# Performance work log

Hardware: AMD Instinct MI355X
Metric: run time of the kernel (lower is better)

The kernel has to match this reference:

```python
import jax, jax.numpy as jnp
import numpy as np

N, E, G = 20000, 320000, 64
IN_DIM, HID, HEADS, NCLS = 512, 256, 2, 10
EPS = 1e-5
SLOPE = 0.2


def setup_inputs() -> dict:
    key = jax.random.key(0)
    ks = jax.random.split(key, 24)
    s = 0.02
    inp = {
        "feat": jax.random.normal(ks[0], (N, IN_DIM), jnp.float32),
        "src": jax.random.randint(ks[1], (E,), 0, N, jnp.int32),
        "dst": jax.random.randint(ks[2], (E,), 0, N, jnp.int32),
        "graph_ids": jnp.sort(jax.random.randint(ks[3], (N,), 0, G, jnp.int32)),
        # GATv2Conv params (fc_src, fc_dst, attn)
        "W_src": jax.random.normal(ks[4], (IN_DIM, HEADS * HID), jnp.float32) * s,
        "b_src": jnp.zeros((HEADS * HID,), jnp.float32),
        "W_dst": jax.random.normal(ks[5], (IN_DIM, HEADS * HID), jnp.float32) * s,
        "b_dst": jnp.zeros((HEADS * HID,), jnp.float32),
        "attn": jax.random.normal(ks[6], (HEADS, HID), jnp.float32) * s,
        # skip_lin: input_dim -> 2*hidden
        "W_skip": jax.random.normal(ks[7], (IN_DIM, 2 * HID), jnp.float32) * s,
        "b_skip": jnp.zeros((2 * HID,), jnp.float32),
        # bn1 affine
        "gamma": jnp.ones((2 * HID,), jnp.float32),
        "beta": jnp.zeros((2 * HID,), jnp.float32),
        # dim_reducer
        "W_red": jax.random.normal(ks[8], (2 * HID, HID), jnp.float32) * s,
        "b_red": jnp.zeros((HID,), jnp.float32),
        # attention-pool gate Linear(hidden, 1)
        "w_gate": jax.random.normal(ks[9], (HID, 1), jnp.float32) * s,
        "b_gate": jnp.zeros((1,), jnp.float32),
        # classifier MLP
        "W1": jax.random.normal(ks[10], (HID, HID // 2), jnp.float32) * s,
        "b1": jnp.zeros((HID // 2,), jnp.float32),
        "W2": jax.random.normal(ks[11], (HID // 2, NCLS), jnp.float32) * s,
        "b2": jnp.zeros((NCLS,), jnp.float32),
    }
    return inp


def _gatv2(feat, src, dst, W_src, b_src, W_dst, b_dst, attn):
    # feat_src/feat_dst: [N, H, D]
    fs = (feat @ W_src + b_src).reshape(N, HEADS, HID)
    fd = (feat @ W_dst + b_dst).reshape(N, HEADS, HID)
    fs_e = fs[src]                               # [E, H, D]
    m = jax.nn.leaky_relu(fs_e + fd[dst], SLOPE)  # [E, H, D]
    e = jnp.einsum("ehd,hd->eh", m, attn)         # [E, H]
    # edge softmax grouped by destination node
    e_max = jax.ops.segment_max(e, dst, num_segments=N)          # [N, H]
    e_exp = jnp.exp(e - e_max[dst])                               # [E, H]
    denom = jax.ops.segment_sum(e_exp, dst, num_segments=N)      # [N, H]
    alpha = e_exp / denom[dst]                                    # [E, H]
    out = jax.ops.segment_sum(alpha[:, :, None] * fs_e, dst, num_segments=N)
    return out  # [N, H, D]; zero rows for zero in-degree nodes


def reference(feat, src, dst, graph_ids, W_src, b_src, W_dst, b_dst, attn,
              W_skip, b_skip, gamma, beta, W_red, b_red, w_gate, b_gate,
              W1, b1, W2, b2):
    h1 = jax.nn.elu(_gatv2(feat, src, dst, W_src, b_src, W_dst, b_dst, attn))
    h1 = h1.reshape(N, HEADS * HID)
    h1 = h1 + (feat @ W_skip + b_skip)
    # BatchNorm1d (training-mode batch statistics, biased variance)
    mu = jnp.mean(h1, axis=0)
    var = jnp.mean((h1 - mu) ** 2, axis=0)
    h1 = (h1 - mu) * jax.lax.rsqrt(var + EPS) * gamma + beta
    hr = h1 @ W_red + b_red                      # [N, HID]
    # GlobalAttentionPooling: segment softmax of gate scores over each graph
    gate = hr @ w_gate + b_gate                  # [N, 1]
    g_max = jax.ops.segment_max(gate, graph_ids, num_segments=G)
    g_exp = jnp.exp(gate - g_max[graph_ids])
    g_den = jax.ops.segment_sum(g_exp, graph_ids, num_segments=G)
    a = g_exp / g_den[graph_ids]                 # [N, 1]
    h_g = jax.ops.segment_sum(a * hr, graph_ids, num_segments=G)  # [G, HID]
    # classifier (dropout = identity at inference)
    return jax.nn.relu(h_g @ W1 + b1) @ W2 + b2  # [G, NCLS]
```

## Files before the change

### kernel.cpp

```cpp
#include <hip/hip_runtime.h>
#include <math.h>

#define N_NODES 20000
#define N_EDGES 320000
#define N_GRAPH 64
#define IN_DIM  512
#define HID     256
#define F2      512
#define EPS_BN  1e-5f
#define SLOPE   0.2f
#define SCAN_BLOCKS 79
#define N_RT    157
#define RT_PAD  20096

typedef unsigned short u16;
typedef __attribute__((ext_vector_type(8))) short bf16x8;
typedef __attribute__((ext_vector_type(4))) float floatx4;

__device__ __forceinline__ u16 bf_hi(float x) {
    unsigned int u = __float_as_uint(x);
    return (u16)((u + 0x7fffu + ((u >> 16) & 1u)) >> 16);
}
__device__ __forceinline__ float bf_val(u16 h) {
    return __uint_as_float((unsigned int)h << 16);
}
__device__ __forceinline__ void unpack2(unsigned int u, float& lo, float& hi) {
    lo = __uint_as_float(u << 16);
    hi = __uint_as_float(u & 0xffff0000u);
}
__device__ __forceinline__ float lr(float x) { return fmaxf(x, SLOPE * x); }

__global__ void init_zero_kernel(int* counts, int* cursor, float* stats,
                                 float* h_gnum, float* gden, float* gate) {
    int i = blockIdx.x * blockDim.x + threadIdx.x;
    if (i < N_NODES) { counts[i] = 0; cursor[i] = 0; gate[i] = 0.f; }
    if (i < 1024) stats[i] = 0.f;
    if (i < N_GRAPH * HID) h_gnum[i] = 0.f;
    if (i < N_GRAPH) gden[i] = 0.f;
}

__global__ __launch_bounds__(256) void split_feat_kernel(
    const float* __restrict__ X, u16* __restrict__ Hi, int total8, int pad8) {
    int i = blockIdx.x * 256 + threadIdx.x;
    if (i >= pad8) return;
    size_t base = (size_t)i * 8;
    if (i >= total8) {
        *(uint4*)(Hi + base) = make_uint4(0, 0, 0, 0);
        return;
    }
    float4 x0 = *(const float4*)(X + base);
    float4 x1 = *(const float4*)(X + base + 4);
    float xs[8] = {x0.x, x0.y, x0.z, x0.w, x1.x, x1.y, x1.z, x1.w};
    union { u16 s[8]; uint4 v; } h;
#pragma unroll
    for (int j = 0; j < 8; j++) h.s[j] = bf_hi(xs[j]);
    *(uint4*)(Hi + base) = h.v;
}

__global__ __launch_bounds__(256) void split_wt_kernel(
    const float* __restrict__ Ws, const float* __restrict__ Wd,
    const float* __restrict__ Wk, const float* __restrict__ Wr,
    u16* __restrict__ Hi, u16* __restrict__ Lo) {
    __shared__ float t[32][33];
    int w = blockIdx.z;
    int ncols = (w == 3) ? 256 : 512;
    int n0 = blockIdx.y * 32;
    if (n0 >= ncols) return;
    const float* W = (w == 0) ? Ws : ((w == 1) ? Wd : ((w == 2) ? Wk : Wr));
    size_t obase = (size_t)w * 512 * 512;
    int k0 = blockIdx.x * 32;
    int tx = threadIdx.x, ty = threadIdx.y;
#pragma unroll
    for (int i = 0; i < 4; i++)
        t[ty * 4 + i][tx] = W[(size_t)(k0 + ty * 4 + i) * ncols + n0 + tx];
    __syncthreads();
#pragma unroll
    for (int i = 0; i < 4; i++) {
        float x = t[tx][ty * 4 + i];
        u16 hh = bf_hi(x);
        size_t o = obase + (size_t)(n0 + ty * 4 + i) * 512 + k0 + tx;
        Hi[o] = hh;
        Lo[o] = bf_hi(x - bf_val(hh));
    }
}

__global__ __launch_bounds__(256) void gemm_mfma_triple(
    const u16* __restrict__ Fhi, const u16* __restrict__ Wthi,
    const float* __restrict__ b_src, const float* __restrict__ b_dst,
    const float* __restrict__ b_skip,
    u16* __restrict__ FS16, u16* __restrict__ FD16,
    u16* __restrict__ h1hi, u16* __restrict__ h1lo) {
    __shared__ u16 As[2][128 * 72];
    int b = blockIdx.x;
    int xcd = b & 7, slot = b >> 3;
    int rt = (slot / 12) * 8 + xcd;
    if (rt >= N_RT) return;
    int cw = slot % 12;
    int w_idx = cw >> 2;
    int col0 = (cw & 3) * 128;
    int row0 = rt * 128;
    int tid = threadIdx.x;
    int lane = tid & 63, wave = tid >> 6;
    int wm = (wave & 1) * 64, wn = (wave >> 1) * 64;
    int quad = lane >> 4, l16 = lane & 15;

    int sr = tid >> 1, sh = (tid & 1) * 32;
    const u16* gA = Fhi + (size_t)(row0 + sr) * 512 + sh;
    int sOff = sr * 72 + sh;

    const u16* Wb = Wthi + (size_t)w_idx * 512 * 512;
    const u16* bP[4];
#pragma unroll
    for (int nt = 0; nt < 4; nt++)
        bP[nt] = Wb + (size_t)(col0 + wn + nt * 16 + l16) * 512 + quad * 8;

    floatx4 acc[4][4];
#pragma unroll
    for (int i = 0; i < 4; i++)
#pragma unroll
        for (int j = 0; j < 4; j++) acc[i][j] = (floatx4){0.f, 0.f, 0.f, 0.f};

    union { uint4 u; bf16x8 v; } bcur[8], bnxt[8];
    {
        uint4 a0 = *(const uint4*)(gA + 0);
        uint4 a1 = *(const uint4*)(gA + 8);
        uint4 a2 = *(const uint4*)(gA + 16);
        uint4 a3 = *(const uint4*)(gA + 24);
#pragma unroll
        for (int nt = 0; nt < 4; nt++) {
            bcur[nt * 2 + 0].u = *(const uint4*)(bP[nt] + 0);
            bcur[nt * 2 + 1].u = *(const uint4*)(bP[nt] + 32);
        }
        *(uint4*)(&As[0][sOff + 0])  = a0;
        *(uint4*)(&As[0][sOff + 8])  = a1;
        *(uint4*)(&As[0][sOff + 16]) = a2;
        *(uint4*)(&As[0][sOff + 24]) = a3;
    }
    __syncthreads();

    for (int kk = 0; kk < 8; kk++) {
        uint4 na0, na1, na2, na3;
        bool more = kk < 7;
        if (more) {
            int k1 = (kk + 1) * 64;
            na0 = *(const uint4*)(gA + k1 + 0);
            na1 = *(const uint4*)(gA + k1 + 8);
            na2 = *(const uint4*)(gA + k1 + 16);
            na3 = *(const uint4*)(gA + k1 + 24);
#pragma unroll
            for (int nt = 0; nt < 4; nt++) {
                bnxt[nt * 2 + 0].u = *(const uint4*)(bP[nt] + k1 + 0);
                bnxt[nt * 2 + 1].u = *(const uint4*)(bP[nt] + k1 + 32);
            }
        }
        const u16* base = &As[kk & 1][0];
#pragma unroll
        for (int s = 0; s < 2; s++) {
#pragma unroll
            for (int mt = 0; mt < 4; mt++) {
                bf16x8 ah = *(const bf16x8*)&base[(wm + mt * 16 + l16) * 72 + s * 32 + quad * 8];
#pragma unroll
                for (int nt = 0; nt < 4; nt++)
                    acc[mt][nt] = __builtin_amdgcn_mfma_f32_16x16x32_bf16(ah, bcur[nt * 2 + s].v, acc[mt][nt], 0, 0, 0);
            }
        }
        if (more) {
            u16* d = &As[(kk + 1) & 1][sOff];
            *(uint4*)(d + 0)  = na0;
            *(uint4*)(d + 8)  = na1;
            *(uint4*)(d + 16) = na2;
            *(uint4*)(d + 24) = na3;
            __syncthreads();
#pragma unroll
            for (int i = 0; i < 8; i++) bcur[i] = bnxt[i];
        }
    }

    const float* bias = (w_idx == 0) ? b_src : ((w_idx == 1) ? b_dst : b_skip);
    float bv[4];
#pragma unroll
    for (int nt = 0; nt < 4; nt++) bv[nt] = bias[col0 + wn + nt * 16 + l16];
#pragma unroll
    for (int mt = 0; mt < 4; mt++) {
#pragma unroll
        for (int r = 0; r < 4; r++) {
            int m = row0 + wm + mt * 16 + quad * 4 + r;
            if (m < N_NODES) {
#pragma unroll
                for (int nt = 0; nt < 4; nt++) {
                    int n = col0 + wn + nt * 16 + l16;
                    float vv = acc[mt][nt][r] + bv[nt];
                    if (w_idx == 0)      FS16[(size_t)m * 512 + n] = bf_hi(vv);
                    else if (w_idx == 1) FD16[(size_t)m * 512 + n] = bf_hi(vv);
                    else {
                        u16 hh = bf_hi(vv);
                        h1hi[(size_t)m * 512 + n] = hh;
                        h1lo[(size_t)m * 512 + n] = bf_hi(vv - bf_val(hh));
                    }
                }
            }
        }
    }
}

__global__ void hist_kernel(const int* __restrict__ dst, int* __restrict__ counts) {
    int e = blockIdx.x * blockDim.x + threadIdx.x;
    if (e < N_EDGES) atomicAdd(&counts[dst[e]], 1);
}

__global__ __launch_bounds__(256) void scan_local_kernel(
    const int* __restrict__ counts, int* __restrict__ row_ptr, int* __restrict__ bsum) {
    __shared__ int buf[256];
    int b = blockIdx.x, tid = threadIdx.x;
    int i = b * 256 + tid;
    buf[tid] = (i < N_NODES) ? counts[i] : 0;
    __syncthreads();
    for (int off = 1; off < 256; off <<= 1) {
        int t = (tid >= off) ? buf[tid - off] : 0;
        __syncthreads();
        buf[tid] += t;
        __syncthreads();
    }
    if (i < N_NODES) row_ptr[i + 1] = buf[tid];
    if (tid == 255) bsum[b] = buf[255];
}

__global__ __launch_bounds__(256) void scan_fixup_kernel(
    const int* __restrict__ bsum, int* __restrict__ row_ptr) {
    __shared__ int red[256];
    int b = blockIdx.x, tid = threadIdx.x;
    red[tid] = (tid < b) ? bsum[tid] : 0;
    __syncthreads();
    for (int off = 128; off > 0; off >>= 1) {
        if (tid < off) red[tid] += red[tid + off];
        __syncthreads();
    }
    int offset = red[0];
    int i = b * 256 + tid;
    if (i < N_NODES) row_ptr[i + 1] += offset;
    if (b == 0 && tid == 0) row_ptr[0] = 0;
}

__global__ void scatter_kernel(const int* __restrict__ src, const int* __restrict__ dst,
                               const int* __restrict__ row_ptr,
                               int* __restrict__ cursor, int* __restrict__ csr_src) {
    int e = blockIdx.x * blockDim.x + threadIdx.x;
    if (e < N_EDGES) {
        int d = dst[e];
        int pos = atomicAdd(&cursor[d], 1);
        csr_src[row_ptr[d] + pos] = src[e];
    }
}

__global__ __launch_bounds__(256) void edge_fused_kernel(
    const u16* __restrict__ FS16, const u16* __restrict__ FD16,
    const float* __restrict__ attn, const int* __restrict__ csr_src,
    const int* __restrict__ row_ptr,
    u16* __restrict__ h1hi, u16* __restrict__ h1lo) {
    __shared__ float red[3 * 512];
    __shared__ float den[2];
    int n = blockIdx.x, tid = threadIdx.x;
    int lane = tid & 63, wave = tid >> 6;
    int beg = row_ptr[n], end = row_ptr[n + 1], deg = end - beg;
    if (tid < 2) den[tid] = 0.f;

    float fdv[8], aw[8];
    {
        uint4 q = *(const uint4*)(FD16 + (size_t)n * 512 + 8 * lane);
        unpack2(q.x, fdv[0], fdv[1]); unpack2(q.y, fdv[2], fdv[3]);
        unpack2(q.z, fdv[4], fdv[5]); unpack2(q.w, fdv[6], fdv[7]);
        float4 a0 = *(const float4*)(attn + 8 * lane);
        float4 a1 = *(const float4*)(attn + 8 * lane + 4);
        aw[0] = a0.x; aw[1] = a0.y; aw[2] = a0.z; aw[3] = a0.w;
        aw[4] = a1.x; aw[5] = a1.y; aw[6] = a1.z; aw[7] = a1.w;
    }
    __syncthreads();

    float acc[8] = {0.f, 0.f, 0.f, 0.f, 0.f, 0.f, 0.f, 0.f};
    float dp = 0.f;
    for (int j = wave; j < deg; j += 4) {
        int s = csr_src[beg + j];
        uint4 q = *(const uint4*)(FS16 + (size_t)s * 512 + 8 * lane);
        float f[8];
        unpack2(q.x, f[0], f[1]); unpack2(q.y, f[2], f[3]);
        unpack2(q.z, f[4], f[5]); unpack2(q.w, f[6], f[7]);
        float p = 0.f;
#pragma unroll
        for (int k = 0; k < 8; k++) p += lr(f[k] + fdv[k]) * aw[k];
#pragma unroll
        for (int off = 16; off > 0; off >>= 1) p += __shfl_xor(p, off, 64);
        float ex = expf(p);
#pragma unroll
        for (int k = 0; k < 8; k++) acc[k] += ex * f[k];
        if ((lane & 31) == 0) dp += ex;
    }
    if ((lane & 31) == 0) atomicAdd(&den[lane >> 5], dp);

    if (wave > 0) {
        float* r = &red[(wave - 1) * 512 + lane * 8];
        *(float4*)(r + 0) = *(float4*)&acc[0];
        *(float4*)(r + 4) = *(float4*)&acc[4];
    }
    __syncthreads();
    if (wave == 0) {
#pragma unroll
        for (int w = 0; w < 3; w++) {
            const float* r = &red[w * 512 + lane * 8];
#pragma unroll
            for (int k = 0; k < 8; k++) acc[k] += r[k];
        }
        float d = (lane < 32) ? den[0] : den[1];
        float inv = d > 0.f ? 1.f / d : 0.f;
        size_t base = (size_t)n * 512 + 8 * lane;
        union { u16 s[8]; uint4 v; } qh, ql;
        qh.v = *(const uint4*)(h1hi + base);
        ql.v = *(const uint4*)(h1lo + base);
#pragma unroll
        for (int k = 0; k < 8; k++) {
            float skip = bf_val(qh.s[k]) + bf_val(ql.s[k]);
            float x = acc[k] * inv;
            x = x > 0.f ? x : expm1f(x);
            float y = x + skip;
            u16 hh = bf_hi(y);
            qh.s[k] = hh;
            ql.s[k] = bf_hi(y - bf_val(hh));
        }
        *(uint4*)(h1hi + base) = qh.v;
        *(uint4*)(h1lo + base) = ql.v;
    }
}

__global__ __launch_bounds__(256) void bn_stats_kernel(const u16* __restrict__ h1hi,
                                                       float* __restrict__ stats,
                                                       int rows_per_block) {
    int tid = threadIdx.x;
    int r0 = blockIdx.x * rows_per_block;
    int r1 = min(r0 + rows_per_block, N_NODES);
    float s0 = 0.f, q0 = 0.f, s1 = 0.f, q1 = 0.f;
    for (int r = r0; r < r1; r++) {
        float a = bf_val(h1hi[(size_t)r * F2 + tid]);
        float b = bf_val(h1hi[(size_t)r * F2 + 256 + tid]);
        s0 += a; q0 += a * a;
        s1 += b; q1 += b * b;
    }
    atomicAdd(&stats[tid], s0);
    atomicAdd(&stats[256 + tid], s1);
    atomicAdd(&stats[512 + tid], q0);
    atomicAdd(&stats[512 + 256 + tid], q1);
}

__global__ void bn_finalize_kernel(const float* __restrict__ stats,
                                   const float* __restrict__ gamma,
                                   const float* __restrict__ beta,
                                   float* __restrict__ bscale, float* __restrict__ bshift) {
    int c = threadIdx.x;
    float mu = stats[c] / (float)N_NODES;
    float var = stats[512 + c] / (float)N_NODES - mu * mu;
    float sc = gamma[c] * rsqrtf(var + EPS_BN);
    bscale[c] = sc;
    bshift[c] = beta[c] - mu * sc;
}

__global__ __launch_bounds__(256) void bn_fold_kernel(
    const u16* __restrict__ Whi3, const u16* __restrict__ Wlo3,
    const float* __restrict__ bscale, const float* __restrict__ bshift,
    const float* __restrict__ b_red,
    u16* __restrict__ Wphi, u16* __restrict__ Wplo, float* __restrict__ bias2) {
    __shared__ float red[256];
    int n = blockIdx.x, tid = threadIdx.x;
    float part = 0.f;
    for (int k = tid; k < 512; k += 256) {
        size_t o = (size_t)n * 512 + k;
        float w = bf_val(Whi3[o]) + bf_val(Wlo3[o]);
        part += bshift[k] * w;
        float wp = w * bscale[k];
        u16 hh = bf_hi(wp);
        Wphi[o] = hh;
        Wplo[o] = bf_hi(wp - bf_val(hh));
    }
    red[tid] = part; __syncthreads();
    for (int off = 128; off > 0; off >>= 1) {
        if (tid < off) red[tid] += red[tid + off];
        __syncthreads();
    }
    if (tid == 0) bias2[n] = b_red[n] + red[0];
}

__global__ __launch_bounds__(256) void gemm_mfma_red(
    const u16* __restrict__ Ahi, const u16* __restrict__ Alo,
    const u16* __restrict__ Bhi, const u16* __restrict__ Blo,
    const float* __restrict__ bias2, const float* __restrict__ wg,
    float* __restrict__ hr, float* __restrict__ gate) {
    __shared__ u16 AsHi[128 * 40];
    __shared__ u16 AsLo[128 * 40];
    int tid = threadIdx.x;
    int row0 = blockIdx.x * 128;
    int col0 = blockIdx.y * 128;
    int lane = tid & 63, wave = tid >> 6;
    int wm = (wave & 1) * 64, wn = (wave >> 1) * 64;
    int quad = lane >> 4, l16 = lane & 15;

    int sr = tid >> 1, sh = (tid & 1) * 16;
    int grow = row0 + sr;
    bool ok = grow < N_NODES;
    u16* sH = &AsHi[sr * 40 + sh];
    u16* sL = &AsLo[sr * 40 + sh];

    const u16* bPh[4];
    const u16* bPl[4];
#pragma unroll
    for (int nt = 0; nt < 4; nt++) {
        size_t o = (size_t)(col0 + wn + nt * 16 + l16) * 512 + quad * 8;
        bPh[nt] = Bhi + o;
        bPl[nt] = Blo + o;
    }

    floatx4 acc[4][4];
#pragma unroll
    for (int i = 0; i < 4; i++)
#pragma unroll
        for (int j = 0; j < 4; j++) acc[i][j] = (floatx4){0.f, 0.f, 0.f, 0.f};

    for (int k0 = 0; k0 < 512; k0 += 32) {
        uint4 h0 = make_uint4(0, 0, 0, 0), h1v = h0, l0 = h0, l1 = h0;
        if (ok) {
            const u16* g = Ahi + (size_t)grow * 512 + k0 + sh;
            const u16* gl = Alo + (size_t)grow * 512 + k0 + sh;
            h0 = *(const uint4*)(g);
            h1v = *(const uint4*)(g + 8);
            l0 = *(const uint4*)(gl);
            l1 = *(const uint4*)(gl + 8);
        }
        union { uint4 u; bf16x8 v; } bh[4], bl[4];
#pragma unroll
        for (int nt = 0; nt < 4; nt++) {
            bh[nt].u = *(const uint4*)(bPh[nt] + k0);
            bl[nt].u = *(const uint4*)(bPl[nt] + k0);
        }
        __syncthreads();
        *(uint4*)(sH + 0) = h0;
        *(uint4*)(sH + 8) = h1v;
        *(uint4*)(sL + 0) = l0;
        *(uint4*)(sL + 8) = l1;
        __syncthreads();
#pragma unroll
        for (int mt = 0; mt < 4; mt++) {
            int me = (wm + mt * 16 + l16) * 40 + quad * 8;
            bf16x8 ah = *(const bf16x8*)&AsHi[me];
            bf16x8 al = *(const bf16x8*)&AsLo[me];
#pragma unroll
            for (int nt = 0; nt < 4; nt++) {
                acc[mt][nt] = __builtin_amdgcn_mfma_f32_16x16x32_bf16(ah, bh[nt].v, acc[mt][nt], 0, 0, 0);
                acc[mt][nt] = __builtin_amdgcn_mfma_f32_16x16x32_bf16(ah, bl[nt].v, acc[mt][nt], 0, 0, 0);
                acc[mt][nt] = __builtin_amdgcn_mfma_f32_16x16x32_bf16(al, bh[nt].v, acc[mt][nt], 0, 0, 0);
            }
        }
    }

    float bv[4], wgv[4];
#pragma unroll
    for (int nt = 0; nt < 4; nt++) {
        int n = col0 + wn + nt * 16 + l16;
        bv[nt] = bias2[n];
        wgv[nt] = wg[n];
    }
#pragma unroll
    for (int mt = 0; mt < 4; mt++) {
#pragma unroll
        for (int r = 0; r < 4; r++) {
            int m = row0 + wm + mt * 16 + quad * 4 + r;
            float vv[4], g = 0.f;
#pragma unroll
            for (int nt = 0; nt < 4; nt++) {
                vv[nt] = acc[mt][nt][r] + bv[nt];
                g += vv[nt] * wgv[nt];
            }
#pragma unroll
            for (int s = 8; s > 0; s >>= 1) g += __shfl_xor(g, s, 64);
            if (m < N_NODES) {
#pragma unroll
                for (int nt = 0; nt < 4; nt++)
                    hr[(size_t)m * HID + col0 + wn + nt * 16 + l16] = vv[nt];
                if (l16 == 0) atomicAdd(&gate[m], g);
            }
        }
    }
}

__device__ __forceinline__ int lower_bound_dev(const int* a, int n, int v) {
    int lo = 0, hi = n;
    while (lo < hi) {
        int mid = (lo + hi) >> 1;
        if (a[mid] < v) lo = mid + 1; else hi = mid;
    }
    return lo;
}

__global__ __launch_bounds__(256) void pool_partial_kernel(
    const float* __restrict__ hr, const float* __restrict__ gate,
    const int* __restrict__ gids, float* __restrict__ h_gnum,
    float* __restrict__ gden) {
    int b = blockIdx.x;
    int g = b >> 3, part = b & 7;
    int tid = threadIdx.x;
    int start = lower_bound_dev(gids, N_NODES, g);
    int end = lower_bound_dev(gids, N_NODES, g + 1);
    int span = end - start;
    int p_beg = start + (span * part) / 8;
    int p_end = start + (span * (part + 1)) / 8;
    if (p_beg >= p_end) return;
    __shared__ float wa[256];
    __shared__ float red[256];
    float acc = 0.f, denacc = 0.f;
    for (int cbeg = p_beg; cbeg < p_end; cbeg += 256) {
        int c = min(256, p_end - cbeg);
        float e = 0.f;
        if (tid < c) { e = expf(gate[cbeg + tid]); wa[tid] = e; }
        red[tid] = (tid < c) ? e : 0.f;
        __syncthreads();
        for (int off = 128; off > 0; off >>= 1) {
            if (tid < off) red[tid] += red[tid + off];
            __syncthreads();
        }
        denacc += red[0];
        for (int i = 0; i < c; i++) acc += wa[i] * hr[(size_t)(cbeg + i) * HID + tid];
        __syncthreads();
    }
    atomicAdd(&h_gnum[g * HID + tid], acc);
    if (tid == 0) atomicAdd(&gden[g], denacc);
}

__global__ __launch_bounds__(128) void classifier_kernel(
    const float* __restrict__ h_gnum, const float* __restrict__ gden,
    const float* __restrict__ W1, const float* __restrict__ b1,
    const float* __restrict__ W2, const float* __restrict__ b2,
    float* __restrict__ out) {
    int g = blockIdx.x;
    int tid = threadIdx.x;
    __shared__ float hg[256];
    __shared__ float z1[128];
    float d = gden[g];
    float invd = d > 0.f ? 1.f / d : 0.f;
    hg[tid] = h_gnum[g * HID + tid] * invd;
    hg[tid + 128] = h_gnum[g * HID + tid + 128] * invd;
    __syncthreads();
    float a = b1[tid];
#pragma unroll 8
    for (int k = 0; k < 256; k++) a += hg[k] * W1[k * 128 + tid];
    z1[tid] = a > 0.f ? a : 0.f;
    __syncthreads();
    if (tid < 10) {
        float o = b2[tid];
#pragma unroll 8
        for (int j = 0; j < 128; j++) o += z1[j] * W2[j * 10 + tid];
        out[g * 10 + tid] = o;
    }
}

extern "C" void kernel_launch(void* const* d_in, const int* in_sizes, int n_in,
                              void* d_out, int out_size, void* d_ws, size_t ws_size,
                              hipStream_t stream) {
    const float* feat   = (const float*)d_in[0];
    const int*   src    = (const int*)d_in[1];
    const int*   dst    = (const int*)d_in[2];
    const int*   gids   = (const int*)d_in[3];
    const float* W_src  = (const float*)d_in[4];
    const float* b_src  = (const float*)d_in[5];
    const float* W_dst  = (const float*)d_in[6];
    const float* b_dst  = (const float*)d_in[7];
    const float* attn   = (const float*)d_in[8];
    const float* W_skip = (const float*)d_in[9];
    const float* b_skip = (const float*)d_in[10];
    const float* gamma  = (const float*)d_in[11];
    const float* beta   = (const float*)d_in[12];
    const float* W_red  = (const float*)d_in[13];
    const float* b_red  = (const float*)d_in[14];
    const float* w_gate = (const float*)d_in[15];
    const float* W1     = (const float*)d_in[17];
    const float* b1     = (const float*)d_in[18];
    const float* W2     = (const float*)d_in[19];
    const float* b2     = (const float*)d_in[20];
    float* out = (float*)d_out;

    char* p = (char*)d_ws;
    auto alloc = [&](size_t bytes) -> char* {
        char* r = p;
        p += (bytes + 255) & ~(size_t)255;
        return r;
    };
    u16*   FS16     = (u16*)alloc((size_t)N_NODES * F2 * 2);
    u16*   FD16     = (u16*)alloc((size_t)N_NODES * F2 * 2);
    u16*   h1hi     = (u16*)alloc((size_t)N_NODES * F2 * 2);
    u16*   h1lo     = (u16*)alloc((size_t)N_NODES * F2 * 2);
    float* gate     = (float*)alloc((size_t)N_NODES * 4);
    float* stats    = (float*)alloc(1024 * 4);
    float* bn_scale = (float*)alloc(512 * 4);
    float* bn_shift = (float*)alloc(512 * 4);
    float* bias2    = (float*)alloc(256 * 4);
    float* h_gnum   = (float*)alloc((size_t)N_GRAPH * HID * 4);
    float* gden     = (float*)alloc((size_t)N_GRAPH * 4);
    int* counts     = (int*)alloc((size_t)N_NODES * 4);
    int* row_ptr    = (int*)alloc((size_t)(N_NODES + 1) * 4);
    int* cursor     = (int*)alloc((size_t)N_NODES * 4);
    int* csr_src    = (int*)alloc((size_t)N_EDGES * 4);
    int* bsum       = (int*)alloc((size_t)SCAN_BLOCKS * 4);
    u16* Fhi        = (u16*)alloc((size_t)RT_PAD * IN_DIM * 2);
    u16* Wthi       = (u16*)alloc((size_t)4 * 512 * 512 * 2);
    u16* Wtlo       = (u16*)alloc((size_t)4 * 512 * 512 * 2);
    u16* Wphi       = (u16*)alloc((size_t)HID * 512 * 2);
    u16* Wplo       = (u16*)alloc((size_t)HID * 512 * 2);
    float* hr = (float*)Fhi;
    (void)ws_size; (void)in_sizes; (void)n_in; (void)out_size;

    const size_t WSZ = (size_t)512 * 512;

    init_zero_kernel<<<(N_NODES + 255) / 256, 256, 0, stream>>>(
        counts, cursor, stats, h_gnum, gden, gate);
    split_feat_kernel<<<(RT_PAD * IN_DIM / 8 + 255) / 256, 256, 0, stream>>>(
        feat, Fhi, N_NODES * IN_DIM / 8, RT_PAD * IN_DIM / 8);
    split_wt_kernel<<<dim3(16, 16, 4), dim3(32, 8), 0, stream>>>(
        W_src, W_dst, W_skip, W_red, Wthi, Wtlo);

    gemm_mfma_triple<<<dim3(((N_RT + 7) / 8) * 8 * 12), 256, 0, stream>>>(
        Fhi, Wthi, b_src, b_dst, b_skip, FS16, FD16, h1hi, h1lo);

    hist_kernel<<<(N_EDGES + 255) / 256, 256, 0, stream>>>(dst, counts);
    scan_local_kernel<<<SCAN_BLOCKS, 256, 0, stream>>>(counts, row_ptr, bsum);
    scan_fixup_kernel<<<SCAN_BLOCKS, 256, 0, stream>>>(bsum, row_ptr);
    scatter_kernel<<<(N_EDGES + 255) / 256, 256, 0, stream>>>(src, dst, row_ptr, cursor, csr_src);

    edge_fused_kernel<<<N_NODES, 256, 0, stream>>>(
        FS16, FD16, attn, csr_src, row_ptr, h1hi, h1lo);

    bn_stats_kernel<<<500, 256, 0, stream>>>(h1hi, stats, 40);
    bn_finalize_kernel<<<1, 512, 0, stream>>>(stats, gamma, beta, bn_scale, bn_shift);
    bn_fold_kernel<<<HID, 256, 0, stream>>>(
        Wthi + 3 * WSZ, Wtlo + 3 * WSZ, bn_scale, bn_shift, b_red, Wphi, Wplo, bias2);

    dim3 g256((N_NODES + 127) / 128, 2);
    gemm_mfma_red<<<g256, 256, 0, stream>>>(
        h1hi, h1lo, Wphi, Wplo, bias2, w_gate, hr, gate);

    pool_partial_kernel<<<N_GRAPH * 8, 256, 0, stream>>>(hr, gate, gids, h_gnum, gden);

    classifier_kernel<<<N_GRAPH, 128, 0, stream>>>(h_gnum, gden, W1, b1, W2, b2, out);
}
```

Baseline: 433.2 us.

## Merge prep/hist launches, fold BN finalize, and vectorize GEMM epilogue stores

Three setup kernels (feature split, weight split, zero-init) become one prep launch, and the edge histogram is appended as extra blocks of the triple GEMM launch. The BN finalize kernel is folded into bn_fold, so every block recomputes scale and shift into shared memory. In both GEMMs the MFMA operands are swapped, which transposes the accumulator layout so each lane holds four consecutive columns and can write them with packed uint2/float4 stores instead of scalar stores. This cuts launch overhead and store transactions, at the cost of the histogram atomics now sharing a launch with the GEMM and some redundant per-block BN math.

```diff
diff --git a/kernel.cpp b/kernel.cpp
--- a/kernel.cpp
+++ b/kernel.cpp
@@ -13,6 +13,13 @@
 #define N_RT    157
 #define RT_PAD  20096
 
+#define SF_BLOCKS   5024
+#define SW_BLOCKS   1024
+#define INIT_BLOCKS 79
+#define PREP_BLOCKS (SF_BLOCKS + SW_BLOCKS + INIT_BLOCKS)
+#define TRIPLE_BLOCKS 1920
+#define HIST_BLOCKS   1250
+
 typedef unsigned short u16;
 typedef __attribute__((ext_vector_type(8))) short bf16x8;
 typedef __attribute__((ext_vector_type(4))) float floatx4;
@@ -30,57 +37,59 @@
 }
 __device__ __forceinline__ float lr(float x) { return fmaxf(x, SLOPE * x); }
 
-__global__ void init_zero_kernel(int* counts, int* cursor, float* stats,
-                                 float* h_gnum, float* gden, float* gate) {
-    int i = blockIdx.x * blockDim.x + threadIdx.x;
-    if (i < N_NODES) { counts[i] = 0; cursor[i] = 0; gate[i] = 0.f; }
-    if (i < 1024) stats[i] = 0.f;
-    if (i < N_GRAPH * HID) h_gnum[i] = 0.f;
-    if (i < N_GRAPH) gden[i] = 0.f;
-}
-
-__global__ __launch_bounds__(256) void split_feat_kernel(
-    const float* __restrict__ X, u16* __restrict__ Hi, int total8, int pad8) {
-    int i = blockIdx.x * 256 + threadIdx.x;
-    if (i >= pad8) return;
-    size_t base = (size_t)i * 8;
-    if (i >= total8) {
-        *(uint4*)(Hi + base) = make_uint4(0, 0, 0, 0);
-        return;
-    }
-    float4 x0 = *(const float4*)(X + base);
-    float4 x1 = *(const float4*)(X + base + 4);
-    float xs[8] = {x0.x, x0.y, x0.z, x0.w, x1.x, x1.y, x1.z, x1.w};
-    union { u16 s[8]; uint4 v; } h;
-#pragma unroll
-    for (int j = 0; j < 8; j++) h.s[j] = bf_hi(xs[j]);
-    *(uint4*)(Hi + base) = h.v;
-}
-
-__global__ __launch_bounds__(256) void split_wt_kernel(
+__global__ __launch_bounds__(256) void prep_kernel(
+    const float* __restrict__ feat, u16* __restrict__ Fhi,
     const float* __restrict__ Ws, const float* __restrict__ Wd,
     const float* __restrict__ Wk, const float* __restrict__ Wr,
-    u16* __restrict__ Hi, u16* __restrict__ Lo) {
+    u16* __restrict__ Whi, u16* __restrict__ Wlo,
+    int* __restrict__ counts, int* __restrict__ cursor,
+    float* __restrict__ stats, float* __restrict__ h_gnum,
+    float* __restrict__ gden, float* __restrict__ gate) {
     __shared__ float t[32][33];
-    int w = blockIdx.z;
-    int ncols = (w == 3) ? 256 : 512;
-    int n0 = blockIdx.y * 32;
-    if (n0 >= ncols) return;
-    const float* W = (w == 0) ? Ws : ((w == 1) ? Wd : ((w == 2) ? Wk : Wr));
-    size_t obase = (size_t)w * 512 * 512;
-    int k0 = blockIdx.x * 32;
-    int tx = threadIdx.x, ty = threadIdx.y;
-#pragma unroll
-    for (int i = 0; i < 4; i++)
-        t[ty * 4 + i][tx] = W[(size_t)(k0 + ty * 4 + i) * ncols + n0 + tx];
-    __syncthreads();
-#pragma unroll
-    for (int i = 0; i < 4; i++) {
-        float x = t[tx][ty * 4 + i];
-        u16 hh = bf_hi(x);
-        size_t o = obase + (size_t)(n0 + ty * 4 + i) * 512 + k0 + tx;
-        Hi[o] = hh;
-        Lo[o] = bf_hi(x - bf_val(hh));
+    int b = blockIdx.x;
+    int tid = threadIdx.x;
+    if (b < SF_BLOCKS) {
+        int i = b * 256 + tid;
+        size_t base = (size_t)i * 8;
+        if (i >= N_NODES * IN_DIM / 8) {
+            *(uint4*)(Fhi + base) = make_uint4(0, 0, 0, 0);
+            return;
+        }
+        float4 x0 = *(const float4*)(feat + base);
+        float4 x1 = *(const float4*)(feat + base + 4);
+        float xs[8] = {x0.x, x0.y, x0.z, x0.w, x1.x, x1.y, x1.z, x1.w};
+        union { u16 s[8]; uint4 v; } h;
+#pragma unroll
+        for (int j = 0; j < 8; j++) h.s[j] = bf_hi(xs[j]);
+        *(uint4*)(Fhi + base) = h.v;
+    } else if (b < SF_BLOCKS + SW_BLOCKS) {
+        int bb = b - SF_BLOCKS;
+        int kx = bb & 15, ny = (bb >> 4) & 15, w = bb >> 8;
+        int ncols = (w == 3) ? 256 : 512;
+        int n0 = ny * 32;
+        if (n0 >= ncols) return;
+        const float* W = (w == 0) ? Ws : ((w == 1) ? Wd : ((w == 2) ? Wk : Wr));
+        size_t obase = (size_t)w * 512 * 512;
+        int k0 = kx * 32;
+        int tx = tid & 31, ty = tid >> 5;
+#pragma unroll
+        for (int i = 0; i < 4; i++)
+            t[ty * 4 + i][tx] = W[(size_t)(k0 + ty * 4 + i) * ncols + n0 + tx];
+        __syncthreads();
+#pragma unroll
+        for (int i = 0; i < 4; i++) {
+            float x = t[tx][ty * 4 + i];
+            u16 hh = bf_hi(x);
+            size_t o = obase + (size_t)(n0 + ty * 4 + i) * 512 + k0 + tx;
+            Whi[o] = hh;
+            Wlo[o] = bf_hi(x - bf_val(hh));
+        }
+    } else {
+        int i = (b - SF_BLOCKS - SW_BLOCKS) * 256 + tid;
+        if (i < N_NODES) { counts[i] = 0; cursor[i] = 0; gate[i] = 0.f; }
+        if (i < 1024) stats[i] = 0.f;
+        if (i < N_GRAPH * HID) h_gnum[i] = 0.f;
+        if (i < N_GRAPH) gden[i] = 0.f;
     }
 }
 
@@ -89,9 +98,15 @@
     const float* __restrict__ b_src, const float* __restrict__ b_dst,
     const float* __restrict__ b_skip,
     u16* __restrict__ FS16, u16* __restrict__ FD16,
-    u16* __restrict__ h1hi, u16* __restrict__ h1lo) {
+    u16* __restrict__ h1hi, u16* __restrict__ h1lo,
+    const int* __restrict__ dst, int* __restrict__ counts) {
     __shared__ u16 As[2][128 * 72];
     int b = blockIdx.x;
+    if (b >= TRIPLE_BLOCKS) {
+        int e = (b - TRIPLE_BLOCKS) * 256 + threadIdx.x;
+        if (e < N_EDGES) atomicAdd(&counts[dst[e]], 1);
+        return;
+    }
     int xcd = b & 7, slot = b >> 3;
     int rt = (slot / 12) * 8 + xcd;
     if (rt >= N_RT) return;
@@ -161,7 +176,8 @@
                 bf16x8 ah = *(const bf16x8*)&base[(wm + mt * 16 + l16) * 72 + s * 32 + quad * 8];
 #pragma unroll
                 for (int nt = 0; nt < 4; nt++)
-                    acc[mt][nt] = __builtin_amdgcn_mfma_f32_16x16x32_bf16(ah, bcur[nt * 2 + s].v, acc[mt][nt], 0, 0, 0);
+                    acc[mt][nt] = __builtin_amdgcn_mfma_f32_16x16x32_bf16(
+                        bcur[nt * 2 + s].v, ah, acc[mt][nt], 0, 0, 0);
             }
         }
         if (more) {
@@ -177,35 +193,37 @@
     }
 
     const float* bias = (w_idx == 0) ? b_src : ((w_idx == 1) ? b_dst : b_skip);
-    float bv[4];
-#pragma unroll
-    for (int nt = 0; nt < 4; nt++) bv[nt] = bias[col0 + wn + nt * 16 + l16];
-#pragma unroll
-    for (int mt = 0; mt < 4; mt++) {
-#pragma unroll
-        for (int r = 0; r < 4; r++) {
-            int m = row0 + wm + mt * 16 + quad * 4 + r;
-            if (m < N_NODES) {
-#pragma unroll
-                for (int nt = 0; nt < 4; nt++) {
-                    int n = col0 + wn + nt * 16 + l16;
-                    float vv = acc[mt][nt][r] + bv[nt];
-                    if (w_idx == 0)      FS16[(size_t)m * 512 + n] = bf_hi(vv);
-                    else if (w_idx == 1) FD16[(size_t)m * 512 + n] = bf_hi(vv);
-                    else {
-                        u16 hh = bf_hi(vv);
-                        h1hi[(size_t)m * 512 + n] = hh;
-                        h1lo[(size_t)m * 512 + n] = bf_hi(vv - bf_val(hh));
-                    }
-                }
+    float4 b4[4];
+#pragma unroll
+    for (int wt = 0; wt < 4; wt++)
+        b4[wt] = *(const float4*)(bias + col0 + wn + wt * 16 + quad * 4);
+#pragma unroll
+    for (int ft = 0; ft < 4; ft++) {
+        int m = row0 + wm + ft * 16 + l16;
+        if (m >= N_NODES) continue;
+        size_t rb = (size_t)m * 512;
+#pragma unroll
+        for (int wt = 0; wt < 4; wt++) {
+            int nb = col0 + wn + wt * 16 + quad * 4;
+            float v0 = acc[ft][wt][0] + b4[wt].x;
+            float v1 = acc[ft][wt][1] + b4[wt].y;
+            float v2 = acc[ft][wt][2] + b4[wt].z;
+            float v3 = acc[ft][wt][3] + b4[wt].w;
+            u16 h0 = bf_hi(v0), h1_ = bf_hi(v1), h2 = bf_hi(v2), h3 = bf_hi(v3);
+            uint2 wv;
+            wv.x = (unsigned)h0 | ((unsigned)h1_ << 16);
+            wv.y = (unsigned)h2 | ((unsigned)h3 << 16);
+            if (w_idx == 0)      *(uint2*)(FS16 + rb + nb) = wv;
+            else if (w_idx == 1) *(uint2*)(FD16 + rb + nb) = wv;
+            else {
+                *(uint2*)(h1hi + rb + nb) = wv;
+                uint2 lv;
+                lv.x = (unsigned)bf_hi(v0 - bf_val(h0)) | ((unsigned)bf_hi(v1 - bf_val(h1_)) << 16);
+                lv.y = (unsigned)bf_hi(v2 - bf_val(h2)) | ((unsigned)bf_hi(v3 - bf_val(h3)) << 16);
+                *(uint2*)(h1lo + rb + nb) = lv;
             }
         }
     }
-}
-
-__global__ void hist_kernel(const int* __restrict__ dst, int* __restrict__ counts) {
-    int e = blockIdx.x * blockDim.x + threadIdx.x;
-    if (e < N_EDGES) atomicAdd(&counts[dst[e]], 1);
 }
 
 __global__ __launch_bounds__(256) void scan_local_kernel(
@@ -349,31 +367,29 @@
     atomicAdd(&stats[512 + 256 + tid], q1);
 }
 
-__global__ void bn_finalize_kernel(const float* __restrict__ stats,
-                                   const float* __restrict__ gamma,
-                                   const float* __restrict__ beta,
-                                   float* __restrict__ bscale, float* __restrict__ bshift) {
-    int c = threadIdx.x;
-    float mu = stats[c] / (float)N_NODES;
-    float var = stats[512 + c] / (float)N_NODES - mu * mu;
-    float sc = gamma[c] * rsqrtf(var + EPS_BN);
-    bscale[c] = sc;
-    bshift[c] = beta[c] - mu * sc;
-}
-
 __global__ __launch_bounds__(256) void bn_fold_kernel(
+    const float* __restrict__ stats, const float* __restrict__ gamma,
+    const float* __restrict__ beta,
     const u16* __restrict__ Whi3, const u16* __restrict__ Wlo3,
-    const float* __restrict__ bscale, const float* __restrict__ bshift,
     const float* __restrict__ b_red,
     u16* __restrict__ Wphi, u16* __restrict__ Wplo, float* __restrict__ bias2) {
+    __shared__ float sScale[512], sShift[512];
     __shared__ float red[256];
     int n = blockIdx.x, tid = threadIdx.x;
+    for (int c = tid; c < 512; c += 256) {
+        float mu = stats[c] / (float)N_NODES;
+        float var = stats[512 + c] / (float)N_NODES - mu * mu;
+        float sc = gamma[c] * rsqrtf(var + EPS_BN);
+        sScale[c] = sc;
+        sShift[c] = beta[c] - mu * sc;
+    }
+    __syncthreads();
     float part = 0.f;
     for (int k = tid; k < 512; k += 256) {
         size_t o = (size_t)n * 512 + k;
         float w = bf_val(Whi3[o]) + bf_val(Wlo3[o]);
-        part += bshift[k] * w;
-        float wp = w * bscale[k];
+        part += sShift[k] * w;
+        float wp = w * sScale[k];
         u16 hh = bf_hi(wp);
         Wphi[o] = hh;
         Wplo[o] = bf_hi(wp - bf_val(hh));
@@ -450,40 +466,38 @@
             bf16x8 al = *(const bf16x8*)&AsLo[me];
 #pragma unroll
             for (int nt = 0; nt < 4; nt++) {
-                acc[mt][nt] = __builtin_amdgcn_mfma_f32_16x16x32_bf16(ah, bh[nt].v, acc[mt][nt], 0, 0, 0);
-                acc[mt][nt] = __builtin_amdgcn_mfma_f32_16x16x32_bf16(ah, bl[nt].v, acc[mt][nt], 0, 0, 0);
-                acc[mt][nt] = __builtin_amdgcn_mfma_f32_16x16x32_bf16(al, bh[nt].v, acc[mt][nt], 0, 0, 0);
+                acc[mt][nt] = __builtin_amdgcn_mfma_f32_16x16x32_bf16(bh[nt].v, ah, acc[mt][nt], 0, 0, 0);
+                acc[mt][nt] = __builtin_amdgcn_mfma_f32_16x16x32_bf16(bl[nt].v, ah, acc[mt][nt], 0, 0, 0);
+                acc[mt][nt] = __builtin_amdgcn_mfma_f32_16x16x32_bf16(bh[nt].v, al, acc[mt][nt], 0, 0, 0);
             }
         }
     }
 
-    float bv[4], wgv[4];
-#pragma unroll
-    for (int nt = 0; nt < 4; nt++) {
-        int n = col0 + wn + nt * 16 + l16;
-        bv[nt] = bias2[n];
-        wgv[nt] = wg[n];
-    }
-#pragma unroll
-    for (int mt = 0; mt < 4; mt++) {
-#pragma unroll
-        for (int r = 0; r < 4; r++) {
-            int m = row0 + wm + mt * 16 + quad * 4 + r;
-            float vv[4], g = 0.f;
-#pragma unroll
-            for (int nt = 0; nt < 4; nt++) {
-                vv[nt] = acc[mt][nt][r] + bv[nt];
-                g += vv[nt] * wgv[nt];
-            }
-#pragma unroll
-            for (int s = 8; s > 0; s >>= 1) g += __shfl_xor(g, s, 64);
-            if (m < N_NODES) {
-#pragma unroll
-                for (int nt = 0; nt < 4; nt++)
-                    hr[(size_t)m * HID + col0 + wn + nt * 16 + l16] = vv[nt];
-                if (l16 == 0) atomicAdd(&gate[m], g);
-            }
-        }
+    float4 b4[4], w4[4];
+#pragma unroll
+    for (int wt = 0; wt < 4; wt++) {
+        int nb = col0 + wn + wt * 16 + quad * 4;
+        b4[wt] = *(const float4*)(bias2 + nb);
+        w4[wt] = *(const float4*)(wg + nb);
+    }
+#pragma unroll
+    for (int ft = 0; ft < 4; ft++) {
+        int m = row0 + wm + ft * 16 + l16;
+        bool ok2 = m < N_NODES;
+        float g = 0.f;
+#pragma unroll
+        for (int wt = 0; wt < 4; wt++) {
+            float4 v;
+            v.x = acc[ft][wt][0] + b4[wt].x;
+            v.y = acc[ft][wt][1] + b4[wt].y;
+            v.z = acc[ft][wt][2] + b4[wt].z;
+            v.w = acc[ft][wt][3] + b4[wt].w;
+            g += v.x * w4[wt].x + v.y * w4[wt].y + v.z * w4[wt].z + v.w * w4[wt].w;
+            if (ok2) *(float4*)(hr + (size_t)m * HID + col0 + wn + wt * 16 + quad * 4) = v;
+        }
+        g += __shfl_xor(g, 16, 64);
+        g += __shfl_xor(g, 32, 64);
+        if (ok2 && lane < 16) atomicAdd(&gate[m], g);
     }
 }
 
@@ -594,8 +608,6 @@
     u16*   h1lo     = (u16*)alloc((size_t)N_NODES * F2 * 2);
     float* gate     = (float*)alloc((size_t)N_NODES * 4);
     float* stats    = (float*)alloc(1024 * 4);
-    float* bn_scale = (float*)alloc(512 * 4);
-    float* bn_shift = (float*)alloc(512 * 4);
     float* bias2    = (float*)alloc(256 * 4);
     float* h_gnum   = (float*)alloc((size_t)N_GRAPH * HID * 4);
     float* gden     = (float*)alloc((size_t)N_GRAPH * 4);
@@ -614,17 +626,13 @@
 
     const size_t WSZ = (size_t)512 * 512;
 
-    init_zero_kernel<<<(N_NODES + 255) / 256, 256, 0, stream>>>(
+    prep_kernel<<<PREP_BLOCKS, 256, 0, stream>>>(
+        feat, Fhi, W_src, W_dst, W_skip, W_red, Wthi, Wtlo,
         counts, cursor, stats, h_gnum, gden, gate);
-    split_feat_kernel<<<(RT_PAD * IN_DIM / 8 + 255) / 256, 256, 0, stream>>>(
-        feat, Fhi, N_NODES * IN_DIM / 8, RT_PAD * IN_DIM / 8);
-    split_wt_kernel<<<dim3(16, 16, 4), dim3(32, 8), 0, stream>>>(
-        W_src, W_dst, W_skip, W_red, Wthi, Wtlo);
-
-    gemm_mfma_triple<<<dim3(((N_RT + 7) / 8) * 8 * 12), 256, 0, stream>>>(
-        Fhi, Wthi, b_src, b_dst, b_skip, FS16, FD16, h1hi, h1lo);
-
-    hist_kernel<<<(N_EDGES + 255) / 256, 256, 0, stream>>>(dst, counts);
+
+    gemm_mfma_triple<<<TRIPLE_BLOCKS + HIST_BLOCKS, 256, 0, stream>>>(
+        Fhi, Wthi, b_src, b_dst, b_skip, FS16, FD16, h1hi, h1lo, dst, counts);
+
     scan_local_kernel<<<SCAN_BLOCKS, 256, 0, stream>>>(counts, row_ptr, bsum);
     scan_fixup_kernel<<<SCAN_BLOCKS, 256, 0, stream>>>(bsum, row_ptr);
     scatter_kernel<<<(N_EDGES + 255) / 256, 256, 0, stream>>>(src, dst, row_ptr, cursor, csr_src);
@@ -633,9 +641,8 @@
         FS16, FD16, attn, csr_src, row_ptr, h1hi, h1lo);
 
     bn_stats_kernel<<<500, 256, 0, stream>>>(h1hi, stats, 40);
-    bn_finalize_kernel<<<1, 512, 0, stream>>>(stats, gamma, beta, bn_scale, bn_shift);
     bn_fold_kernel<<<HID, 256, 0, stream>>>(
-        Wthi + 3 * WSZ, Wtlo + 3 * WSZ, bn_scale, bn_shift, b_red, Wphi, Wplo, bias2);
+        stats, gamma, beta, Wthi + 3 * WSZ, Wtlo + 3 * WSZ, b_red, Wphi, Wplo, bias2);
 
     dim3 g256((N_NODES + 127) / 128, 2);
     gemm_mfma_red<<<g256, 256, 0, stream>>>(
```

New measurement: 403.8 us. 6.8% less time.
